# Kernel optimization log

Hardware: AMD Instinct MI355X
Metric: run time of the kernel (lower is better)

Reference implementation:

```python
import jax, jax.numpy as jnp
import numpy as np

B, S, D, H = 2, 2048, 2048, 16
HD = D // H  # 128


def setup_inputs() -> dict:
    key = jax.random.key(0)
    ks = jax.random.split(key, 7)
    x = jax.random.normal(ks[0], (B, S, D), jnp.float32)
    # 4 tree-position components per token (e.g. depth/branch coordinates)
    pos = jax.random.uniform(ks[1], (B, S, 4), jnp.float32, 0.0, 64.0)
    # tree/causal additive mask: 0 where attending is allowed, -1e9 otherwise
    causal = jnp.where(jnp.tril(jnp.ones((S, S), bool)), 0.0, -1e9).astype(jnp.float32)
    mask = jnp.broadcast_to(causal, (B, S, S))
    scale = D ** -0.5
    wq = jax.random.normal(ks[2], (D, D), jnp.float32) * scale
    wk = jax.random.normal(ks[3], (D, D), jnp.float32) * scale
    wv = jax.random.normal(ks[4], (D, D), jnp.float32) * scale
    wo = jax.random.normal(ks[5], (D, D), jnp.float32) * scale
    return {"x": x, "pos": pos, "mask": mask, "wq": wq, "wk": wk, "wv": wv, "wo": wo}


def reference(x, pos, mask, wq, wk, wv, wo):
    b, s, d = x.shape
    hd = HD
    # theta_of_dims: 1/10000^(arange(0,hd,8)[:hd//8]/hd) -> [hd//8]
    theta = 1.0 / (10000.0 ** (jnp.arange(0, hd, 8)[: hd // 8].astype(jnp.float32) / hd))
    q = (x @ wq.T).reshape(b, s, H, hd)
    k = (x @ wk.T).reshape(b, s, H, hd)
    v = (x @ wv.T).reshape(b, s, H, hd)
    # freqs: [b, s, hd//8, 4] flattened to [b, s, 1, hd//2]
    freqs = jnp.einsum('bij,k->bikj', pos, theta).reshape(b, s, 1, hd // 2)
    cos, sin = jnp.cos(freqs), jnp.sin(freqs)

    def rope(t):
        tr, ti = t[..., 0::2], t[..., 1::2]  # complex pairs (even=real, odd=imag)
        out_r = tr * cos - ti * sin
        out_i = tr * sin + ti * cos
        return jnp.stack([out_r, out_i], axis=-1).reshape(t.shape)

    q, k = rope(q), rope(k)
    scores = jnp.einsum('bqhd,bkhd->bhqk', q, k) / np.float32(np.sqrt(hd))
    scores = scores + mask[:, None, :, :]
    attn = jax.nn.softmax(scores, axis=-1)
    out = jnp.einsum('bhqk,bkhd->bqhd', attn, v).reshape(b, s, d)
    return out @ wo.T
```

## Files before the change

kernel.cpp:

```cpp
#include <hip/hip_runtime.h>
#include <cstdint>
#include <type_traits>

typedef __attribute__((ext_vector_type(8))) short short8;
typedef __attribute__((ext_vector_type(4))) float floatx4;

#define NB 2
#define NS 2048
#define ND 2048
#define NH 16
#define NHD 128

__device__ __forceinline__ float b2f(short s) {
  unsigned u = ((unsigned)(unsigned short)s) << 16;
  return __builtin_bit_cast(float, u);
}
__device__ __forceinline__ short f2b(float f) {
  unsigned u = __builtin_bit_cast(unsigned, f);
  unsigned r = (u + 0x7fffu + ((u >> 16) & 1u)) >> 16;
  return (short)(unsigned short)r;
}

__global__ void cast_all(const float* __restrict__ x, const float* __restrict__ wq,
                         const float* __restrict__ wk, const float* __restrict__ wv,
                         const float* __restrict__ wo, short* __restrict__ dst) {
  const int i = blockIdx.x * blockDim.x + threadIdx.x;
  const float* src;
  int off;
  if (i < 2097152) { src = x;  off = i; }
  else if (i < 3145728) { src = wq; off = i - 2097152; }
  else if (i < 4194304) { src = wk; off = i - 3145728; }
  else if (i < 5242880) { src = wv; off = i - 4194304; }
  else { src = wo; off = i - 5242880; }
  float4 v = ((const float4*)src)[off];
  short4 o;
  o.x = f2b(v.x); o.y = f2b(v.y); o.z = f2b(v.z); o.w = f2b(v.w);
  ((short4*)dst)[i] = o;
}

__device__ __forceinline__ void gld_lds16(const void* g, void* l) {
  __builtin_amdgcn_global_load_lds((const __attribute__((address_space(1))) void*)g,
                                   (__attribute__((address_space(3))) void*)l,
                                   16, 0, 0);
}

__global__ __launch_bounds__(256) void qkv_gemm(const short* __restrict__ A,
                                                const short* __restrict__ Bt,
                                                short* __restrict__ Qh,
                                                short* __restrict__ Kh,
                                                short* __restrict__ vlin) {
  constexpr int K = 2048;
  __shared__ short As[128 * 64];
  __shared__ short Bs[128 * 64];
  const int m0 = blockIdx.y * 128, n0 = blockIdx.x * 128;
  const int which = n0 >> 11;
  const int nl0 = n0 & 2047;
  const int t = threadIdx.x;
  const int wave = t >> 6, lane = t & 63, l15 = lane & 15, quad = lane >> 4;
  const int wm = (wave >> 1) * 64, wn = (wave & 1) * 64;

  floatx4 acc[4][4] = {};

  const int srow = t >> 3;
  const int scol = (t & 7) ^ (srow & 7);
  const short* Ag = A + (long)(m0 + srow) * K + scol * 8;
  const short* Bg = Bt + (long)(n0 + srow) * K + scol * 8;
  char* AsB = (char*)As;
  char* BsB = (char*)Bs;
  const int ldsOff = wave * 1024;

  for (int kt = 0; kt < K; kt += 64) {
#pragma unroll
    for (int i = 0; i < 4; ++i) {
      gld_lds16(Ag + kt + (long)(32 * i) * K, AsB + ldsOff + i * 4096);
      gld_lds16(Bg + kt + (long)(32 * i) * K, BsB + ldsOff + i * 4096);
    }
    __syncthreads();

#pragma unroll
    for (int half = 0; half < 2; ++half) {
      short8 a[4], b[4];
#pragma unroll
      for (int mi = 0; mi < 4; ++mi) {
        const int rr = wm + mi * 16 + l15;
        a[mi] = *(const short8*)&As[rr * 64 + (((half << 2) | quad) ^ (rr & 7)) * 8];
      }
#pragma unroll
      for (int ni = 0; ni < 4; ++ni) {
        const int rr = wn + ni * 16 + l15;
        b[ni] = *(const short8*)&Bs[rr * 64 + (((half << 2) | quad) ^ (rr & 7)) * 8];
      }
#pragma unroll
      for (int mi = 0; mi < 4; ++mi)
#pragma unroll
        for (int ni = 0; ni < 4; ++ni)
          acc[mi][ni] = __builtin_amdgcn_mfma_f32_16x16x32_bf16(a[mi], b[ni], acc[mi][ni], 0, 0, 0);
    }
    __syncthreads();
  }

  short* headDst = (which == 0) ? Qh : Kh;
#pragma unroll
  for (int mi = 0; mi < 4; ++mi) {
#pragma unroll
    for (int ni = 0; ni < 4; ++ni) {
#pragma unroll
      for (int r = 0; r < 4; ++r) {
        const int row = m0 + wm + mi * 16 + quad * 4 + r;
        const int col = nl0 + wn + ni * 16 + l15;
        const short v = f2b(acc[mi][ni][r]);
        if (which == 2) {
          vlin[(long)row * 2048 + col] = v;
        } else {
          const int bb = row >> 11, s = row & 2047, h = col >> 7, hd = col & 127;
          headDst[(((long)(bb * 16 + h) * 2048) + s) * 128 + hd] = v;
        }
      }
    }
  }
}

__global__ __launch_bounds__(256) void gemm_out(const short* __restrict__ A,
                                                const short* __restrict__ Bt,
                                                float* __restrict__ Cout) {
  constexpr int K = 2048, N = 2048;
  __shared__ short As[128 * 64];
  __shared__ short Bs[128 * 64];
  const int m0 = blockIdx.y * 128, n0 = blockIdx.x * 128;
  const int t = threadIdx.x;
  const int wave = t >> 6, lane = t & 63, l15 = lane & 15, quad = lane >> 4;
  const int wm = (wave >> 1) * 64, wn = (wave & 1) * 64;

  floatx4 acc[4][4] = {};

  const int srow = t >> 3;
  const int scol = (t & 7) ^ (srow & 7);
  const short* Ag = A + (long)(m0 + srow) * K + scol * 8;
  const short* Bg = Bt + (long)(n0 + srow) * K + scol * 8;
  char* AsB = (char*)As;
  char* BsB = (char*)Bs;
  const int ldsOff = wave * 1024;

  for (int kt = 0; kt < K; kt += 64) {
#pragma unroll
    for (int i = 0; i < 4; ++i) {
      gld_lds16(Ag + kt + (long)(32 * i) * K, AsB + ldsOff + i * 4096);
      gld_lds16(Bg + kt + (long)(32 * i) * K, BsB + ldsOff + i * 4096);
    }
    __syncthreads();

#pragma unroll
    for (int half = 0; half < 2; ++half) {
      short8 a[4], b[4];
#pragma unroll
      for (int mi = 0; mi < 4; ++mi) {
        const int rr = wm + mi * 16 + l15;
        a[mi] = *(const short8*)&As[rr * 64 + (((half << 2) | quad) ^ (rr & 7)) * 8];
      }
#pragma unroll
      for (int ni = 0; ni < 4; ++ni) {
        const int rr = wn + ni * 16 + l15;
        b[ni] = *(const short8*)&Bs[rr * 64 + (((half << 2) | quad) ^ (rr & 7)) * 8];
      }
#pragma unroll
      for (int mi = 0; mi < 4; ++mi)
#pragma unroll
        for (int ni = 0; ni < 4; ++ni)
          acc[mi][ni] = __builtin_amdgcn_mfma_f32_16x16x32_bf16(a[mi], b[ni], acc[mi][ni], 0, 0, 0);
    }
    __syncthreads();
  }

#pragma unroll
  for (int mi = 0; mi < 4; ++mi)
#pragma unroll
    for (int ni = 0; ni < 4; ++ni)
#pragma unroll
      for (int r = 0; r < 4; ++r) {
        const int row = m0 + wm + mi * 16 + quad * 4 + r;
        const int col = n0 + wn + ni * 16 + l15;
        Cout[(long)row * N + col] = acc[mi][ni][r];
      }
}

__global__ __launch_bounds__(256) void rope_vtrans(short* __restrict__ Qh,
                                                   short* __restrict__ Kh,
                                                   const float* __restrict__ pos,
                                                   const short* __restrict__ v_lin,
                                                   short* __restrict__ Vt) {
  __shared__ short tile[64 * 72];
  const int bx = blockIdx.x;
  if (bx < 4096) {
    const int tid = bx * 256 + threadIdx.x;
    const int kk = tid & 15;
    const int h = (tid >> 4) & 15;
    const int token = tid >> 8;
    const int bb = token >> 11, s = token & 2047;
    const float4 p4 = ((const float4*)pos)[token];
    const float pv[4] = {p4.x, p4.y, p4.z, p4.w};
    const float theta = exp2f(-(float)kk * 0.8304820237218406f);
    const long base = (((long)(bb * 16 + h)) * 2048 + s) * 128 + kk * 8;
    short8 q8 = *(short8*)(Qh + base);
    short8 k8 = *(short8*)(Kh + base);
    short8 qo, ko;
#pragma unroll
    for (int jj = 0; jj < 4; ++jj) {
      const float fr = pv[jj] * theta;
      float sn, c;
      __sincosf(fr, &sn, &c);
      {
        const float tr = b2f(q8[2 * jj]), ti = b2f(q8[2 * jj + 1]);
        qo[2 * jj] = f2b(tr * c - ti * sn);
        qo[2 * jj + 1] = f2b(tr * sn + ti * c);
      }
      {
        const float tr = b2f(k8[2 * jj]), ti = b2f(k8[2 * jj + 1]);
        ko[2 * jj] = f2b(tr * c - ti * sn);
        ko[2 * jj + 1] = f2b(tr * sn + ti * c);
      }
    }
    *(short8*)(Qh + base) = qo;
    *(short8*)(Kh + base) = ko;
  } else {
    const int b2 = bx - 4096;
    const int s0 = (b2 & 31) * 64;
    const int hd0 = ((b2 >> 5) & 1) * 64;
    const int bh = b2 >> 6;
    const int bb = bh >> 4, h = bh & 15;
    const int t = threadIdx.x;
#pragma unroll
    for (int i = 0; i < 2; ++i) {
      const int ch = t + i * 256;
      const int r = ch >> 3, c = ch & 7;
      *(short8*)&tile[r * 72 + c * 8] =
          *(const short8*)(v_lin + (long)(bb * 2048 + s0 + r) * 2048 + h * 128 + hd0 + c * 8);
    }
    __syncthreads();
#pragma unroll
    for (int i = 0; i < 2; ++i) {
      const int ch = t + i * 256;
      const int r2 = ch >> 3, c2 = ch & 7;
      short8 o;
#pragma unroll
      for (int u = 0; u < 8; ++u) o[u] = tile[(c2 * 8 + u) * 72 + r2];
      *(short8*)(Vt + ((long)(bh * 128 + hd0 + r2)) * 2048 + s0 + c2 * 8) = o;
    }
  }
}

__global__ __launch_bounds__(256, 3) void flash(const short* __restrict__ Qh,
                                                const short* __restrict__ Kh,
                                                const short* __restrict__ Vt,
                                                short* __restrict__ ao) {
  __shared__ short Ks[64 * 128];
  __shared__ short Vts[128 * 64];
  __shared__ short Ps[4 * 16 * 64];
  const int id = blockIdx.x;
  const int hi = id >> 8, lo = id & 255;
  const int q0 = lo & 31, bl = lo >> 5;
  const int qt = (hi & 1) ? 31 - q0 : q0;
  const int bh = bl + (hi << 3);
  const int t = threadIdx.x, wave = t >> 6, lane = t & 63, l15 = lane & 15, quad = lane >> 4;
  const int sqb = qt * 64;
  const int lastkt = qt;

  const short* Qbase = Qh + (long)bh * 2048 * 128;
  short8 aq[4];
#pragma unroll
  for (int ks = 0; ks < 4; ++ks)
    aq[ks] = *(const short8*)(Qbase + (long)(sqb + wave * 16 + l15) * 128 + ks * 32 + quad * 8);

  const short* KgBase = Kh + (long)bh * 2048 * 128;
  const short* VgBase = Vt + (long)bh * 128 * 2048;

  short8 kreg[4], vreg[4];
#pragma unroll
  for (int i = 0; i < 4; ++i) {
    const int ch = t + i * 256;
    kreg[i] = *(const short8*)(KgBase + (long)(ch >> 4) * 128 + (ch & 15) * 8);
    vreg[i] = *(const short8*)(VgBase + (long)(ch >> 3) * 2048 + (ch & 7) * 8);
  }

  float l_part[4] = {};
  floatx4 acc_o[8] = {};
  const float CEXP = 0.12751745f;

  for (int kt = 0; kt <= lastkt; ++kt) {
    const int k0 = kt * 64;
    if (kt > 0) __syncthreads();

#pragma unroll
    for (int i = 0; i < 4; ++i) {
      const int ch = t + i * 256;
      const int kr = ch >> 4, kc = ch & 15;
      *(short8*)&Ks[kr * 128 + (((kc & 7) ^ (kr & 7)) | (kc & 8)) * 8] = kreg[i];
      const int vr = ch >> 3, vc = ch & 7;
      *(short8*)&Vts[vr * 64 + (vc ^ (vr & 7)) * 8] = vreg[i];
    }
    __syncthreads();

    if (kt < lastkt) {
      const short* Kg = KgBase + (long)(k0 + 64) * 128;
      const short* Vg = VgBase + (k0 + 64);
#pragma unroll
      for (int i = 0; i < 4; ++i) {
        const int ch = t + i * 256;
        kreg[i] = *(const short8*)(Kg + (long)(ch >> 4) * 128 + (ch & 15) * 8);
        vreg[i] = *(const short8*)(Vg + (long)(ch >> 3) * 2048 + (ch & 7) * 8);
      }
    }

    const bool dg = (kt == lastkt);
    floatx4 accs[4] = {};
    __builtin_amdgcn_s_setprio(1);
#pragma unroll
    for (int ks = 0; ks < 4; ++ks) {
#pragma unroll
      for (int ni = 0; ni < 4; ++ni) {
        const int rr = ni * 16 + l15;
        const int c = ks * 4 + quad;
        const short8 bk = *(const short8*)&Ks[rr * 128 + (((c & 7) ^ (rr & 7)) | (c & 8)) * 8];
        accs[ni] = __builtin_amdgcn_mfma_f32_16x16x32_bf16(aq[ks], bk, accs[ni], 0, 0, 0);
      }
    }
    __builtin_amdgcn_s_setprio(0);
#pragma unroll
    for (int r = 0; r < 4; ++r) {
      const int qrow = sqb + wave * 16 + quad * 4 + r;
      const int prow = quad * 4 + r;
#pragma unroll
      for (int ni = 0; ni < 4; ++ni) {
        float e = exp2f(accs[ni][r] * CEXP);
        if (dg && (k0 + ni * 16 + l15) > qrow) e = 0.f;
        const int pc = ni * 2 + (l15 >> 3);
        Ps[wave * 1024 + prow * 64 + (pc ^ (prow & 7)) * 8 + (l15 & 7)] = f2b(e);
        l_part[r] += e;
      }
    }
    __builtin_amdgcn_s_setprio(1);
#pragma unroll
    for (int ks2 = 0; ks2 < 2; ++ks2) {
      const int pc = ks2 * 4 + quad;
      const short8 ap = *(const short8*)&Ps[wave * 1024 + l15 * 64 + (pc ^ (l15 & 7)) * 8];
#pragma unroll
      for (int nh = 0; nh < 8; ++nh) {
        const int vr = nh * 16 + l15;
        const short8 bv = *(const short8*)&Vts[vr * 64 + (pc ^ (vr & 7)) * 8];
        acc_o[nh] = __builtin_amdgcn_mfma_f32_16x16x32_bf16(ap, bv, acc_o[nh], 0, 0, 0);
      }
    }
    __builtin_amdgcn_s_setprio(0);
  }

  const int bb = bh >> 4, h = bh & 15;
#pragma unroll
  for (int r = 0; r < 4; ++r) {
    float rs = l_part[r];
#pragma unroll
    for (int mm = 8; mm >= 1; mm >>= 1) rs += __shfl_xor(rs, mm, 16);
    const float inv = 1.0f / rs;
    const int s = sqb + wave * 16 + quad * 4 + r;
    const long rowbase = ((long)(bb * 2048 + s)) * 2048 + h * 128;
#pragma unroll
    for (int nh = 0; nh < 8; ++nh) ao[rowbase + nh * 16 + l15] = f2b(acc_o[nh][r] * inv);
  }
}

extern "C" void kernel_launch(void* const* d_in, const int* in_sizes, int n_in,
                              void* d_out, int out_size, void* d_ws, size_t ws_size,
                              hipStream_t stream) {
  const float* x = (const float*)d_in[0];
  const float* pos = (const float*)d_in[1];
  const float* wq = (const float*)d_in[3];
  const float* wk = (const float*)d_in[4];
  const float* wv = (const float*)d_in[5];
  const float* wo = (const float*)d_in[6];
  float* out = (float*)d_out;

  char* ws = (char*)d_ws;
  const size_t MB = 1024 * 1024;
  short* xb    = (short*)(ws + 0);
  short* wqkvb = (short*)(ws + 16 * MB);
  short* wob   = (short*)(ws + 40 * MB);
  short* Qh    = (short*)(ws + 48 * MB);
  short* Kh    = (short*)(ws + 64 * MB);
  short* Vt    = (short*)(ws + 80 * MB);
  short* vlin  = (short*)(ws + 96 * MB);
  short* ao    = (short*)(ws + 96 * MB);

  cast_all<<<24576, 256, 0, stream>>>(x, wq, wk, wv, wo, xb);

  qkv_gemm<<<dim3(48, 32), 256, 0, stream>>>(xb, wqkvb, Qh, Kh, vlin);

  rope_vtrans<<<6144, 256, 0, stream>>>(Qh, Kh, pos, vlin, Vt);

  flash<<<1024, 256, 0, stream>>>(Qh, Kh, Vt, ao);

  gemm_out<<<dim3(16, 32), 256, 0, stream>>>(ao, wob, out);
}
```

Baseline: 422.6 us.

## Split flash attention KV loop across two wave groups with LDS reduction

The flash kernel now launches 512 threads per block. Two groups of four waves each process alternating 64-key tiles for the same query tile, and their partial outputs and row sums are combined through shared memory at the end. Block order is changed to schedule the longest causal query tiles first. This roughly halves the serial KV loop length per block and spreads causal load imbalance better. In exchange it uses more LDS (80KB) per block, adds a final reduction and extra syncs, and may lower the number of resident blocks.

```diff
diff --git a/kernel.cpp b/kernel.cpp
--- a/kernel.cpp
+++ b/kernel.cpp
@@ -248,19 +248,27 @@
   }
 }
 
-__global__ __launch_bounds__(256, 3) void flash(const short* __restrict__ Qh,
+__global__ __launch_bounds__(512, 4) void flash(const short* __restrict__ Qh,
                                                 const short* __restrict__ Kh,
                                                 const short* __restrict__ Vt,
                                                 short* __restrict__ ao) {
-  __shared__ short Ks[64 * 128];
-  __shared__ short Vts[128 * 64];
-  __shared__ short Ps[4 * 16 * 64];
+  __shared__ __align__(16) char smem[81920];
+  short* KsB  = (short*)smem;
+  short* VtsB = (short*)(smem + 32768);
+  short* PsB  = (short*)(smem + 65536);
+  float* accS = (float*)smem;
+  float* lS   = (float*)(smem + 32768);
+
   const int id = blockIdx.x;
-  const int hi = id >> 8, lo = id & 255;
-  const int q0 = lo & 31, bl = lo >> 5;
-  const int qt = (hi & 1) ? 31 - q0 : q0;
-  const int bh = bl + (hi << 3);
-  const int t = threadIdx.x, wave = t >> 6, lane = t & 63, l15 = lane & 15, quad = lane >> 4;
+  const int qt = 31 - (id >> 5);
+  const int bh = id & 31;
+  const int t = threadIdx.x;
+  const int wave = t >> 6, lane = t & 63, l15 = lane & 15, quad = lane >> 4;
+  const int grp = wave >> 2, wv = wave & 3;
+  const int tg = t & 255;
+  short* Ks  = KsB + grp * (64 * 128);
+  short* Vts = VtsB + grp * (128 * 64);
+  short* Ps  = PsB + wave * 1024;
   const int sqb = qt * 64;
   const int lastkt = qt;
 
@@ -268,30 +276,34 @@
   short8 aq[4];
 #pragma unroll
   for (int ks = 0; ks < 4; ++ks)
-    aq[ks] = *(const short8*)(Qbase + (long)(sqb + wave * 16 + l15) * 128 + ks * 32 + quad * 8);
+    aq[ks] = *(const short8*)(Qbase + (long)(sqb + wv * 16 + l15) * 128 + ks * 32 + quad * 8);
 
   const short* KgBase = Kh + (long)bh * 2048 * 128;
   const short* VgBase = Vt + (long)bh * 128 * 2048;
 
-  short8 kreg[4], vreg[4];
-#pragma unroll
-  for (int i = 0; i < 4; ++i) {
-    const int ch = t + i * 256;
-    kreg[i] = *(const short8*)(KgBase + (long)(ch >> 4) * 128 + (ch & 15) * 8);
-    vreg[i] = *(const short8*)(VgBase + (long)(ch >> 3) * 2048 + (ch & 7) * 8);
+  short8 kreg[4] = {}, vreg[4] = {};
+  if (grp <= lastkt) {
+#pragma unroll
+    for (int i = 0; i < 4; ++i) {
+      const int ch = tg + i * 256;
+      kreg[i] = *(const short8*)(KgBase + (long)(grp * 64 + (ch >> 4)) * 128 + (ch & 15) * 8);
+      vreg[i] = *(const short8*)(VgBase + (long)(ch >> 3) * 2048 + grp * 64 + (ch & 7) * 8);
+    }
   }
 
   float l_part[4] = {};
   floatx4 acc_o[8] = {};
   const float CEXP = 0.12751745f;
 
-  for (int kt = 0; kt <= lastkt; ++kt) {
-    const int k0 = kt * 64;
-    if (kt > 0) __syncthreads();
+  for (int kt2 = 0; kt2 <= lastkt; kt2 += 2) {
+    const int my_kt = kt2 + grp;
+    const bool active = my_kt <= lastkt;
+    const int k0 = my_kt * 64;
+    if (kt2 > 0) __syncthreads();
 
 #pragma unroll
     for (int i = 0; i < 4; ++i) {
-      const int ch = t + i * 256;
+      const int ch = tg + i * 256;
       const int kr = ch >> 4, kc = ch & 15;
       *(short8*)&Ks[kr * 128 + (((kc & 7) ^ (kr & 7)) | (kc & 8)) * 8] = kreg[i];
       const int vr = ch >> 3, vc = ch & 7;
@@ -299,70 +311,93 @@
     }
     __syncthreads();
 
-    if (kt < lastkt) {
-      const short* Kg = KgBase + (long)(k0 + 64) * 128;
-      const short* Vg = VgBase + (k0 + 64);
+    if (my_kt + 2 <= lastkt) {
+      const short* Kg = KgBase + (long)(my_kt + 2) * 64 * 128;
+      const short* Vg = VgBase + (my_kt + 2) * 64;
 #pragma unroll
       for (int i = 0; i < 4; ++i) {
-        const int ch = t + i * 256;
+        const int ch = tg + i * 256;
         kreg[i] = *(const short8*)(Kg + (long)(ch >> 4) * 128 + (ch & 15) * 8);
         vreg[i] = *(const short8*)(Vg + (long)(ch >> 3) * 2048 + (ch & 7) * 8);
       }
     }
 
-    const bool dg = (kt == lastkt);
-    floatx4 accs[4] = {};
-    __builtin_amdgcn_s_setprio(1);
-#pragma unroll
-    for (int ks = 0; ks < 4; ++ks) {
-#pragma unroll
-      for (int ni = 0; ni < 4; ++ni) {
-        const int rr = ni * 16 + l15;
-        const int c = ks * 4 + quad;
-        const short8 bk = *(const short8*)&Ks[rr * 128 + (((c & 7) ^ (rr & 7)) | (c & 8)) * 8];
-        accs[ni] = __builtin_amdgcn_mfma_f32_16x16x32_bf16(aq[ks], bk, accs[ni], 0, 0, 0);
-      }
-    }
-    __builtin_amdgcn_s_setprio(0);
+    if (active) {
+      const bool dg = (my_kt == lastkt);
+      floatx4 accs[4] = {};
+      __builtin_amdgcn_s_setprio(1);
+#pragma unroll
+      for (int ks = 0; ks < 4; ++ks) {
+#pragma unroll
+        for (int ni = 0; ni < 4; ++ni) {
+          const int rr = ni * 16 + l15;
+          const int c = ks * 4 + quad;
+          const short8 bk = *(const short8*)&Ks[rr * 128 + (((c & 7) ^ (rr & 7)) | (c & 8)) * 8];
+          accs[ni] = __builtin_amdgcn_mfma_f32_16x16x32_bf16(aq[ks], bk, accs[ni], 0, 0, 0);
+        }
+      }
+      __builtin_amdgcn_s_setprio(0);
+#pragma unroll
+      for (int r = 0; r < 4; ++r) {
+        const int qrow = sqb + wv * 16 + quad * 4 + r;
+        const int prow = quad * 4 + r;
+#pragma unroll
+        for (int ni = 0; ni < 4; ++ni) {
+          float e = exp2f(accs[ni][r] * CEXP);
+          if (dg && (k0 + ni * 16 + l15) > qrow) e = 0.f;
+          const int pc = ni * 2 + (l15 >> 3);
+          Ps[prow * 64 + (pc ^ (prow & 7)) * 8 + (l15 & 7)] = f2b(e);
+          l_part[r] += e;
+        }
+      }
+      __builtin_amdgcn_s_setprio(1);
+#pragma unroll
+      for (int ks2 = 0; ks2 < 2; ++ks2) {
+        const int pc = ks2 * 4 + quad;
+        const short8 ap = *(const short8*)&Ps[l15 * 64 + (pc ^ (l15 & 7)) * 8];
+#pragma unroll
+        for (int nh = 0; nh < 8; ++nh) {
+          const int vr = nh * 16 + l15;
+          const short8 bv = *(const short8*)&Vts[vr * 64 + (pc ^ (vr & 7)) * 8];
+          acc_o[nh] = __builtin_amdgcn_mfma_f32_16x16x32_bf16(ap, bv, acc_o[nh], 0, 0, 0);
+        }
+      }
+      __builtin_amdgcn_s_setprio(0);
+    }
+  }
+
+  __syncthreads();
+  if (grp == 1) {
+#pragma unroll
+    for (int nh = 0; nh < 8; ++nh)
+#pragma unroll
+      for (int r = 0; r < 4; ++r)
+        accS[((nh * 4 + r) * 4 + wv) * 64 + lane] = acc_o[nh][r];
+#pragma unroll
+    for (int r = 0; r < 4; ++r) lS[(r * 4 + wv) * 64 + lane] = l_part[r];
+  }
+  __syncthreads();
+  if (grp == 0) {
+#pragma unroll
+    for (int nh = 0; nh < 8; ++nh)
+#pragma unroll
+      for (int r = 0; r < 4; ++r)
+        acc_o[nh][r] += accS[((nh * 4 + r) * 4 + wv) * 64 + lane];
+#pragma unroll
+    for (int r = 0; r < 4; ++r) l_part[r] += lS[(r * 4 + wv) * 64 + lane];
+
+    const int bb = bh >> 4, h = bh & 15;
 #pragma unroll
     for (int r = 0; r < 4; ++r) {
-      const int qrow = sqb + wave * 16 + quad * 4 + r;
-      const int prow = quad * 4 + r;
-#pragma unroll
-      for (int ni = 0; ni < 4; ++ni) {
-        float e = exp2f(accs[ni][r] * CEXP);
-        if (dg && (k0 + ni * 16 + l15) > qrow) e = 0.f;
-        const int pc = ni * 2 + (l15 >> 3);
-        Ps[wave * 1024 + prow * 64 + (pc ^ (prow & 7)) * 8 + (l15 & 7)] = f2b(e);
-        l_part[r] += e;
-      }
-    }
-    __builtin_amdgcn_s_setprio(1);
-#pragma unroll
-    for (int ks2 = 0; ks2 < 2; ++ks2) {
-      const int pc = ks2 * 4 + quad;
-      const short8 ap = *(const short8*)&Ps[wave * 1024 + l15 * 64 + (pc ^ (l15 & 7)) * 8];
-#pragma unroll
-      for (int nh = 0; nh < 8; ++nh) {
-        const int vr = nh * 16 + l15;
-        const short8 bv = *(const short8*)&Vts[vr * 64 + (pc ^ (vr & 7)) * 8];
-        acc_o[nh] = __builtin_amdgcn_mfma_f32_16x16x32_bf16(ap, bv, acc_o[nh], 0, 0, 0);
-      }
-    }
-    __builtin_amdgcn_s_setprio(0);
-  }
-
-  const int bb = bh >> 4, h = bh & 15;
-#pragma unroll
-  for (int r = 0; r < 4; ++r) {
-    float rs = l_part[r];
-#pragma unroll
-    for (int mm = 8; mm >= 1; mm >>= 1) rs += __shfl_xor(rs, mm, 16);
-    const float inv = 1.0f / rs;
-    const int s = sqb + wave * 16 + quad * 4 + r;
-    const long rowbase = ((long)(bb * 2048 + s)) * 2048 + h * 128;
-#pragma unroll
-    for (int nh = 0; nh < 8; ++nh) ao[rowbase + nh * 16 + l15] = f2b(acc_o[nh][r] * inv);
+      float rs = l_part[r];
+#pragma unroll
+      for (int mm = 8; mm >= 1; mm >>= 1) rs += __shfl_xor(rs, mm, 16);
+      const float inv = 1.0f / rs;
+      const int s = sqb + wv * 16 + quad * 4 + r;
+      const long rowbase = ((long)(bb * 2048 + s)) * 2048 + h * 128;
+#pragma unroll
+      for (int nh = 0; nh < 8; ++nh) ao[rowbase + nh * 16 + l15] = f2b(acc_o[nh][r] * inv);
+    }
   }
 }
 
@@ -394,7 +429,7 @@
 
   rope_vtrans<<<6144, 256, 0, stream>>>(Qh, Kh, pos, vlin, Vt);
 
-  flash<<<1024, 256, 0, stream>>>(Qh, Kh, Vt, ao);
+  flash<<<1024, 512, 0, stream>>>(Qh, Kh, Vt, ao);
 
   gemm_out<<<dim3(16, 32), 256, 0, stream>>>(ao, wob, out);
 }
```

Result: slower. 527.2 us (+24.7%).
